# Kernel tuning notes

Measured on AMD Instinct MI355X. Metric: run time of the kernel, lower is better.

## Reference

```python
import jax, jax.numpy as jnp
import numpy as np

KH, KW = 2, 2  # kernel_size; stride == kernel_size (default), pad == 0 for this config

def setup_inputs() -> dict:
    key = jax.random.key(0)
    k1, k2 = jax.random.split(key)
    B, C, H, W = 32, 64, 64, 64
    nH, nW = H // KH, W // KW
    L = nH * nW                     # 1024
    n = KH * KW * C                 # 256 (grouping = in_feature)
    x = jax.random.normal(k1, (B, C, H, W), dtype=jnp.float32)
    stdv = 6.0 / np.sqrt(n * n / 1.0) ** 0.5  # placeholder, recomputed below
    stdv = 6.0 / np.sqrt(float(n * n) / 1.0) if False else 6.0 / np.sqrt(float(n) * float(n) / float(n)) / 1.0
    stdv = 6.0 / np.sqrt(float(n * n))  # numel // L == n*n -> stdv = 6/sqrt(n*n) = 6/n
    weight = jax.random.uniform(k2, (L, n, n), dtype=jnp.float32, minval=-stdv, maxval=stdv)
    bias = jnp.zeros((1, 1, n, L), dtype=jnp.float32)
    return {"x": x, "weight": weight, "bias": bias}

def reference(x, weight, bias):
    # PointConv with kernel=(2,2), stride=(2,2), pad=0, grouping=C.
    B, C, H, W = x.shape
    nH, nW = H // KH, W // KW
    L = nH * nW
    n = C * KH * KW
    # F.unfold (non-overlapping, stride==kernel): channel order (c, kh, kw), L order (ph, pw)
    patches = x.reshape(B, C, nH, KH, nW, KW).transpose(0, 1, 3, 5, 2, 4).reshape(B, n, L)
    p = patches.reshape(B, 1, n, L)  # (B, C//grouping=1, n, L)
    # per-location matmul: distinct [n,n] weight per spatial patch l
    m = jnp.einsum('bcnl,lnp->bcpl', p, weight) + bias  # (B,1,n,L)
    m = m.reshape(B, C, KH, KW, nH, nW)
    # F.fold inverse of the unfold above
    out = m.transpose(0, 1, 4, 2, 5, 3).reshape(B, C, H, W)
    return out
```

## Files before the change

### kernel.cpp

```cpp
#include <hip/hip_runtime.h>


#define B_  32
#define C_  64
#define H_  64
#define W_  64
#define L_  1024
#define N_  256
#define SA  264

typedef __bf16 bf16x8 __attribute__((ext_vector_type(8)));
typedef float  f32x4  __attribute__((ext_vector_type(4)));

__device__ __forceinline__ unsigned short f2bf(float f) {
  unsigned int u = __builtin_bit_cast(unsigned int, f);
  u += 0x7FFFu + ((u >> 16) & 1u);
  return (unsigned short)(u >> 16);
}

__global__ __launch_bounds__(256, 4) void pointconv_kernel(
    const float* __restrict__ x, const float* __restrict__ wgt,
    const float* __restrict__ bias, float* __restrict__ out) {
  __shared__ unsigned short A[B_ * SA];

  const int bid = blockIdx.x;
  const int l  = ((bid & 7) << 7) | (bid >> 3);
  const int ph = l >> 5, pw = l & 31;
  const int h0 = ph * 2, w0 = pw * 2;

  const int tid = threadIdx.x;

  {
    const int b  = tid & 31;
    const int c0 = tid >> 5;
#pragma unroll
    for (int i = 0; i < 8; ++i) {
      const int c = c0 + i * 8;
      const float* px = x + (((b * C_ + c) * H_ + h0) * W_ + w0);
      float2 v0 = *(const float2*)px;
      float2 v1 = *(const float2*)(px + W_);
      ushort4 q;
      q.x = f2bf(v0.x); q.y = f2bf(v0.y);
      q.z = f2bf(v1.x); q.w = f2bf(v1.y);
      *(ushort4*)&A[b * SA + c * 4] = q;
    }
  }
  __syncthreads();

  const int lane = tid & 63;
  const int wv   = tid >> 6;
  const int col  = lane & 15;
  const int quad = lane >> 4;

  f32x4 acc[2][4];
#pragma unroll
  for (int nt = 0; nt < 4; ++nt) {
    const int p = wv * 64 + nt * 16 + col;
    const float bv = bias[p * L_ + l];
#pragma unroll
    for (int mt = 0; mt < 2; ++mt) {
      acc[mt][nt][0] = bv; acc[mt][nt][1] = bv;
      acc[mt][nt][2] = bv; acc[mt][nt][3] = bv;
    }
  }

  const float* __restrict__ wl = wgt + (size_t)l * (N_ * N_);

#pragma unroll 1
  for (int k0 = 0; k0 < 256; k0 += 32) {
    bf16x8 af[2];
#pragma unroll
    for (int mt = 0; mt < 2; ++mt)
      af[mt] = *(const bf16x8*)&A[(mt * 16 + col) * SA + k0 + quad * 8];

#pragma unroll
    for (int nt = 0; nt < 4; ++nt) {
      const int p = wv * 64 + nt * 16 + col;
      const float* wp = wl + (k0 + quad * 8) * N_ + p;
      union { unsigned short s[8]; bf16x8 v; } bu;
#pragma unroll
      for (int j = 0; j < 8; ++j)
        bu.s[j] = f2bf(wp[j * N_]);
#pragma unroll
      for (int mt = 0; mt < 2; ++mt)
        acc[mt][nt] = __builtin_amdgcn_mfma_f32_16x16x32_bf16(
            af[mt], bu.v, acc[mt][nt], 0, 0, 0);
    }
  }

#pragma unroll
  for (int mt = 0; mt < 2; ++mt) {
#pragma unroll
    for (int nt = 0; nt < 4; ++nt) {
      const int p  = wv * 64 + nt * 16 + col;
      const int c  = p >> 2;
      const int kh = (p >> 1) & 1;
      const int kw = p & 1;
      float* po = out + (((0 * C_ + c) * H_ + h0 + kh) * W_ + w0 + kw);
#pragma unroll
      for (int r = 0; r < 4; ++r) {
        const int b = mt * 16 + quad * 4 + r;
        po[b * (C_ * H_ * W_)] = acc[mt][nt][r];
      }
    }
  }
}

extern "C" void kernel_launch(void* const* d_in, const int* in_sizes, int n_in,
                              void* d_out, int out_size, void* d_ws, size_t ws_size,
                              hipStream_t stream) {
  const float* x    = (const float*)d_in[0];
  const float* wgt  = (const float*)d_in[1];
  const float* bias = (const float*)d_in[2];
  float* out = (float*)d_out;
  pointconv_kernel<<<dim3(L_), dim3(256), 0, stream>>>(x, wgt, bias, out);
}
```

Baseline: 448.1 us.

## Stage weight tiles through LDS with register prefetch and vectorized loads

Weights were previously read as scalar strided global loads per lane and converted to bf16 in the MFMA loop. Now each thread loads 16-byte vectors of the next 32-row weight chunk into registers, converts and writes them to a padded LDS tile, and prefetches the following chunk while the MFMAs run. This coalesces the dominant weight stream (256 MB total) and overlaps its latency, at the cost of extra LDS, two barriers per k-step, more registers, and lower occupancy (launch bounds 4 to 3).

```diff
diff --git a/kernel.cpp b/kernel.cpp
--- a/kernel.cpp
+++ b/kernel.cpp
@@ -8,6 +8,7 @@
 #define L_  1024
 #define N_  256
 #define SA  264
+#define PW  268
 
 typedef __bf16 bf16x8 __attribute__((ext_vector_type(8)));
 typedef float  f32x4  __attribute__((ext_vector_type(4)));
@@ -18,17 +19,28 @@
   return (unsigned short)(u >> 16);
 }
 
-__global__ __launch_bounds__(256, 4) void pointconv_kernel(
+__global__ __launch_bounds__(256, 3) void pointconv_kernel(
     const float* __restrict__ x, const float* __restrict__ wgt,
     const float* __restrict__ bias, float* __restrict__ out) {
   __shared__ unsigned short A[B_ * SA];
+  __shared__ unsigned short WS[32 * PW];
 
   const int bid = blockIdx.x;
   const int l  = ((bid & 7) << 7) | (bid >> 3);
   const int ph = l >> 5, pw = l & 31;
   const int h0 = ph * 2, w0 = pw * 2;
+  const int tid = threadIdx.x;
 
-  const int tid = threadIdx.x;
+  const float* __restrict__ wl = wgt + (size_t)l * (N_ * N_);
+
+  const int kb = (tid >> 6) * 8;
+  const int pq = (tid & 63) * 4;
+  const float* wbase = wl + kb * N_ + pq;
+
+  f32x4 wreg[8];
+#pragma unroll
+  for (int i = 0; i < 8; ++i)
+    wreg[i] = *(const f32x4*)(wbase + i * N_);
 
   {
     const int b  = tid & 31;
@@ -45,7 +57,6 @@
       *(ushort4*)&A[b * SA + c * 4] = q;
     }
   }
-  __syncthreads();
 
   const int lane = tid & 63;
   const int wv   = tid >> 6;
@@ -64,10 +75,24 @@
     }
   }
 
-  const float* __restrict__ wl = wgt + (size_t)l * (N_ * N_);
+#pragma unroll 1
+  for (int k0 = 0; k0 < N_; k0 += 32) {
+#pragma unroll
+    for (int i = 0; i < 8; ++i) {
+      ushort4 q;
+      q.x = f2bf(wreg[i][0]); q.y = f2bf(wreg[i][1]);
+      q.z = f2bf(wreg[i][2]); q.w = f2bf(wreg[i][3]);
+      *(ushort4*)&WS[(kb + i) * PW + pq] = q;
+    }
+    __syncthreads();
 
-#pragma unroll 1
-  for (int k0 = 0; k0 < 256; k0 += 32) {
+    if (k0 + 32 < N_) {
+      const float* nb = wbase + (k0 + 32) * N_;
+#pragma unroll
+      for (int i = 0; i < 8; ++i)
+        wreg[i] = *(const f32x4*)(nb + i * N_);
+    }
+
     bf16x8 af[2];
 #pragma unroll
     for (int mt = 0; mt < 2; ++mt)
@@ -76,16 +101,16 @@
 #pragma unroll
     for (int nt = 0; nt < 4; ++nt) {
       const int p = wv * 64 + nt * 16 + col;
-      const float* wp = wl + (k0 + quad * 8) * N_ + p;
       union { unsigned short s[8]; bf16x8 v; } bu;
 #pragma unroll
       for (int j = 0; j < 8; ++j)
-        bu.s[j] = f2bf(wp[j * N_]);
+        bu.s[j] = WS[(quad * 8 + j) * PW + p];
 #pragma unroll
       for (int mt = 0; mt < 2; ++mt)
         acc[mt][nt] = __builtin_amdgcn_mfma_f32_16x16x32_bf16(
             af[mt], bu.v, acc[mt][nt], 0, 0, 0);
     }
+    __syncthreads();
   }
 
 #pragma unroll
@@ -96,7 +121,7 @@
       const int c  = p >> 2;
       const int kh = (p >> 1) & 1;
       const int kw = p & 1;
-      float* po = out + (((0 * C_ + c) * H_ + h0 + kh) * W_ + w0 + kw);
+      float* po = out + (((c * H_) + h0 + kh) * W_ + w0 + kw);
 #pragma unroll
       for (int r = 0; r < 4; ++r) {
         const int b = mt * 16 + quad * 4 + r;
```

Measured after the change: 417.7 us. 1.07x faster.
